# Kernel optimization log

Measured on AMD Instinct MI355X. Metric: run time of the kernel, lower is better.

## Reference

```python
import jax, jax.numpy as jnp
import numpy as np

N_HEAD = 16


def setup_inputs() -> dict:
    key = jax.random.key(0)
    ks = jax.random.split(key, 11)
    B, T, D = 8, 448, 1024
    init = 0.02
    x = jax.random.normal(ks[0], (B, T, D), dtype=jnp.float32)
    k_cache = jax.random.normal(ks[1], (B, T, D), dtype=jnp.float32)
    v_cache = jax.random.normal(ks[2], (B, T, D), dtype=jnp.float32)
    # Whisper-style additive causal mask: 0 on/below diagonal, large negative above
    mask = jnp.triu(jnp.full((T, T), -1e9, dtype=jnp.float32), k=1)
    Wq = jax.random.normal(ks[3], (D, D), dtype=jnp.float32) * init
    bq = jax.random.normal(ks[4], (D,), dtype=jnp.float32) * init
    Wk = jax.random.normal(ks[5], (D, D), dtype=jnp.float32) * init  # key proj has no bias
    Wv = jax.random.normal(ks[6], (D, D), dtype=jnp.float32) * init
    bv = jax.random.normal(ks[7], (D,), dtype=jnp.float32) * init
    Wo = jax.random.normal(ks[8], (D, D), dtype=jnp.float32) * init
    bo = jax.random.normal(ks[9], (D,), dtype=jnp.float32) * init
    return {"x": x, "k_cache": k_cache, "v_cache": v_cache, "mask": mask,
            "Wq": Wq, "bq": bq, "Wk": Wk, "Wv": Wv, "bv": bv, "Wo": Wo, "bo": bo}


def reference(x, k_cache, v_cache, mask, Wq, bq, Wk, Wv, bv, Wo, bo):
    # QKV projections (key has no bias, as in Whisper)
    q = x @ Wq + bq
    k = x @ Wk
    v = x @ Wv + bv
    # In-place KV cache append: write new keys/values into the tail of the cache
    T_new = k.shape[1]
    k_cache = k_cache.at[:, -T_new:, :].set(k)
    v_cache = v_cache.at[:, -T_new:, :].set(v)

    B, T, D = q.shape
    H = N_HEAD
    dh = D // H
    scale = dh ** (-0.25)  # applied to BOTH q and k

    qh = (q * scale).reshape(B, T, H, dh).transpose(0, 2, 1, 3)           # [B,H,T,dh]
    kh = (k_cache * scale).reshape(B, k_cache.shape[1], H, dh).transpose(0, 2, 1, 3)
    vh = v_cache.reshape(B, v_cache.shape[1], H, dh).transpose(0, 2, 1, 3)

    qk = jnp.einsum('bhqd,bhkd->bhqk', qh, kh) + mask[:T, :T]             # [B,H,T,Tc]
    qk = qk.astype(jnp.float32)  # upcast for softmax, matching original
    w = jax.nn.softmax(qk, axis=-1).astype(q.dtype)

    out = jnp.einsum('bhqk,bhkd->bhqd', w, vh)                            # [B,H,T,dh]
    out = out.transpose(0, 2, 1, 3).reshape(B, T, D)
    return out @ Wo + bo, k_cache, v_cache
```

## Files before the change

kernel.cpp:

```cpp
#include <hip/hip_runtime.h>
#include <hip/hip_bf16.h>
#include <math.h>

#define B 8
#define T 448
#define D 1024
#define H 16
#define DH 64
#define M (B*T)

typedef short short8 __attribute__((ext_vector_type(8)));
typedef float floatx4 __attribute__((ext_vector_type(4)));
typedef unsigned short u16;

__device__ __forceinline__ u16 f2bf(float f) {
    union { float f; unsigned u; } v; v.f = f;
    unsigned r = v.u + 0x7FFF + ((v.u >> 16) & 1);
    return (u16)(r >> 16);
}

__device__ __forceinline__ void gload16(const void* gptr, void* lptr) {
    __builtin_amdgcn_global_load_lds(
        (const __attribute__((address_space(1))) void*)gptr,
        (__attribute__((address_space(3))) void*)lptr, 16, 0, 0);
}

__global__ __launch_bounds__(256) void xconv(const float* __restrict__ x, u16* __restrict__ xb) {
    const int i = blockIdx.x * 256 + threadIdx.x;
    float4 v = ((const float4*)x)[i];
    ushort4 o;
    o.x = f2bf(v.x); o.y = f2bf(v.y); o.z = f2bf(v.z); o.w = f2bf(v.w);
    ((ushort4*)xb)[i] = o;
}

__global__ __launch_bounds__(256) void wconv4(
    const float* __restrict__ Wq, const float* __restrict__ Wk,
    const float* __restrict__ Wv, const float* __restrict__ Wo,
    u16* __restrict__ wt)
{
    __shared__ float tile[64][65];
    const int z = blockIdx.z;
    const float* W = (z == 0) ? Wq : (z == 1) ? Wk : (z == 2) ? Wv : Wo;
    u16* Wt = wt + (size_t)z * D * D;
    const int k0 = blockIdx.y * 64, n0 = blockIdx.x * 64;
    const int tr = threadIdx.x >> 4, tc = threadIdx.x & 15;
    #pragma unroll
    for (int i = 0; i < 4; ++i) {
        float4 v = *(const float4*)(W + (size_t)(k0 + tr + 16 * i) * D + n0 + tc * 4);
        tile[tr + 16 * i][tc * 4 + 0] = v.x;
        tile[tr + 16 * i][tc * 4 + 1] = v.y;
        tile[tr + 16 * i][tc * 4 + 2] = v.z;
        tile[tr + 16 * i][tc * 4 + 3] = v.w;
    }
    __syncthreads();
    #pragma unroll
    for (int i = 0; i < 4; ++i) {
        const int n = tr + 16 * i;
        ushort4 o;
        o.x = f2bf(tile[tc * 4 + 0][n]);
        o.y = f2bf(tile[tc * 4 + 1][n]);
        o.z = f2bf(tile[tc * 4 + 2][n]);
        o.w = f2bf(tile[tc * 4 + 3][n]);
        *(ushort4*)(Wt + (size_t)(n0 + n) * D + k0 + tc * 4) = o;
    }
}

__global__ __launch_bounds__(256) void gemm128(
    const u16* __restrict__ A, const u16* __restrict__ Bt, int mode,
    const float* __restrict__ bq, const float* __restrict__ bv,
    u16* __restrict__ qkvb, float* __restrict__ kout, float* __restrict__ vout,
    u16* __restrict__ vbT,
    const float* __restrict__ bo, float* __restrict__ outp)
{
    __shared__ u16 As[128][32];
    __shared__ u16 Bs[128][32];
    const int m0 = blockIdx.y * 128;
    const int n0 = blockIdx.x * 128;
    const int tid = threadIdx.x;
    const int wave = tid >> 6, lane = tid & 63;
    const int wy = wave >> 1, wx = wave & 1;
    const int lrow = lane & 15, lquad = lane >> 4;

    floatx4 acc[4][4];
    #pragma unroll
    for (int i = 0; i < 4; ++i)
        #pragma unroll
        for (int j = 0; j < 4; ++j)
            acc[i][j] = (floatx4){0.f, 0.f, 0.f, 0.f};

    const u16* agp0 = A + (size_t)(m0 + (tid >> 2)) * 1024 + (tid & 3) * 8;
    const u16* agp1 = agp0 + (size_t)64 * 1024;
    const u16* bgp0 = Bt + (size_t)(n0 + (tid >> 2)) * 1024 + (tid & 3) * 8;
    const u16* bgp1 = bgp0 + (size_t)64 * 1024;
    char* lA0 = (char*)&As[0][0] + wave * 1024;
    char* lA1 = lA0 + 4096;
    char* lB0 = (char*)&Bs[0][0] + wave * 1024;
    char* lB1 = lB0 + 4096;

    for (int k0 = 0; k0 < 1024; k0 += 32) {
        __syncthreads();
        gload16(agp0 + k0, lA0);
        gload16(agp1 + k0, lA1);
        gload16(bgp0 + k0, lB0);
        gload16(bgp1 + k0, lB1);
        __syncthreads();
        short8 af[4], bfr[4];
        #pragma unroll
        for (int i = 0; i < 4; ++i)
            af[i] = *(const short8*)&As[wy * 64 + i * 16 + lrow][lquad * 8];
        #pragma unroll
        for (int j = 0; j < 4; ++j)
            bfr[j] = *(const short8*)&Bs[wx * 64 + j * 16 + lrow][lquad * 8];
        #pragma unroll
        for (int i = 0; i < 4; ++i)
            #pragma unroll
            for (int j = 0; j < 4; ++j)
                acc[i][j] = __builtin_amdgcn_mfma_f32_16x16x32_bf16(af[i], bfr[j], acc[i][j], 0, 0, 0);
    }

    const int sec = (mode == 0) ? (n0 >> 10) : 3;
    #pragma unroll
    for (int j = 0; j < 4; ++j) {
        const int col = n0 + wx * 64 + j * 16 + lrow;
        float bb;
        if (mode == 1) bb = bo[col];
        else bb = (sec == 0) ? bq[col] : (sec == 2 ? bv[col - 2048] : 0.f);
        #pragma unroll
        for (int i = 0; i < 4; ++i) {
            #pragma unroll
            for (int r = 0; r < 4; ++r) {
                const int row = m0 + wy * 64 + i * 16 + lquad * 4 + r;
                const float v = acc[i][j][r] + bb;
                if (mode == 1) {
                    outp[(size_t)row * 1024 + col] = v;
                } else if (sec == 0) {
                    qkvb[(size_t)row * 3072 + col] = f2bf(v);
                } else if (sec == 1) {
                    qkvb[(size_t)row * 3072 + col] = f2bf(v);
                    kout[(size_t)row * 1024 + col - 1024] = v;
                } else {
                    vout[(size_t)row * 1024 + col - 2048] = v;
                    const int bidx = row / 448, tt = row - bidx * 448;
                    vbT[((size_t)bidx * 1024 + (col - 2048)) * 448 + tt] = f2bf(v);
                }
            }
        }
    }
}

__global__ __launch_bounds__(256) void flash_attn(
    const u16* __restrict__ QKVb,
    const u16* __restrict__ VbT,
    u16* __restrict__ Ob)
{
    __shared__ u16 Qs[64][72];
    __shared__ u16 Ks[64][72];
    __shared__ u16 Vt[64][72];
    __shared__ u16 Pt[4][16][72];
    const int qt = blockIdx.x;
    const int bh = blockIdx.y;
    const int h = bh & (H - 1), b = bh >> 4;
    const int tid = threadIdx.x, wave = tid >> 6, lane = tid & 63;
    const int lrow = lane & 15, lquad = lane >> 4;
    const int q0 = qt * 64;

    const u16* qbase = QKVb + (size_t)b * T * 3072 + (size_t)h * DH;
    const u16* kbase = qbase + 1024;
    const u16* vtb   = VbT + (size_t)bh * DH * T;

    {
        const int s = tid * 2;
        short8 v0 = *(const short8*)(qbase + (size_t)(q0 + (s >> 3)) * 3072 + (s & 7) * 8);
        short8 v1 = *(const short8*)(qbase + (size_t)(q0 + ((s + 1) >> 3)) * 3072 + ((s + 1) & 7) * 8);
        *(short8*)&Qs[s >> 3][(s & 7) * 8] = v0;
        *(short8*)&Qs[(s + 1) >> 3][((s + 1) & 7) * 8] = v1;
    }
    __syncthreads();
    short8 aq0 = *(const short8*)&Qs[wave * 16 + lrow][lquad * 8];
    short8 aq1 = *(const short8*)&Qs[wave * 16 + lrow][32 + lquad * 8];

    float m_i[4], l_i[4];
    floatx4 oacc[4];
    #pragma unroll
    for (int r = 0; r < 4; ++r) { m_i[r] = -INFINITY; l_i[r] = 0.f; }
    #pragma unroll
    for (int n = 0; n < 4; ++n) oacc[n] = (floatx4){0.f, 0.f, 0.f, 0.f};

    const float SC = 0.125f * 1.44269504088896340736f;
    const int nkt = qt + 1;

    for (int kt = 0; kt < nkt; ++kt) {
        const int k0 = kt * 64;
        {
            const int s = tid * 2;
            const int r0 = s >> 3, o0 = (s & 7) * 8;
            const int r1 = (s + 1) >> 3, o1 = ((s + 1) & 7) * 8;
            short8 kv0 = *(const short8*)(kbase + (size_t)(k0 + r0) * 3072 + o0);
            short8 kv1 = *(const short8*)(kbase + (size_t)(k0 + r1) * 3072 + o1);
            short8 vv0 = *(const short8*)(vtb + (size_t)r0 * T + k0 + o0);
            short8 vv1 = *(const short8*)(vtb + (size_t)r1 * T + k0 + o1);
            __syncthreads();
            *(short8*)&Ks[r0][o0] = kv0;
            *(short8*)&Ks[r1][o1] = kv1;
            *(short8*)&Vt[r0][o0] = vv0;
            *(short8*)&Vt[r1][o1] = vv1;
        }
        __syncthreads();

        floatx4 s4[4];
        #pragma unroll
        for (int sub = 0; sub < 4; ++sub) {
            short8 bk0 = *(const short8*)&Ks[sub * 16 + lrow][lquad * 8];
            short8 bk1 = *(const short8*)&Ks[sub * 16 + lrow][32 + lquad * 8];
            floatx4 z = (floatx4){0.f, 0.f, 0.f, 0.f};
            z = __builtin_amdgcn_mfma_f32_16x16x32_bf16(aq0, bk0, z, 0, 0, 0);
            z = __builtin_amdgcn_mfma_f32_16x16x32_bf16(aq1, bk1, z, 0, 0, 0);
            s4[sub] = z;
        }

        float p[4][4];
        #pragma unroll
        for (int r = 0; r < 4; ++r) {
            const int qg = q0 + wave * 16 + lquad * 4 + r;
            float sv[4];
            float mx = -INFINITY;
            #pragma unroll
            for (int sub = 0; sub < 4; ++sub) {
                const int kk = k0 + sub * 16 + lrow;
                float v = s4[sub][r] * SC;
                v = (kk <= qg) ? v : -INFINITY;
                sv[sub] = v;
                mx = fmaxf(mx, v);
            }
            mx = fmaxf(mx, __shfl_xor(mx, 1));
            mx = fmaxf(mx, __shfl_xor(mx, 2));
            mx = fmaxf(mx, __shfl_xor(mx, 4));
            mx = fmaxf(mx, __shfl_xor(mx, 8));
            const float mnew = fmaxf(m_i[r], mx);
            const float alpha = exp2f(m_i[r] - mnew);
            float ls = 0.f;
            #pragma unroll
            for (int sub = 0; sub < 4; ++sub) {
                const float pv = exp2f(sv[sub] - mnew);
                p[sub][r] = pv;
                ls += pv;
            }
            ls += __shfl_xor(ls, 1);
            ls += __shfl_xor(ls, 2);
            ls += __shfl_xor(ls, 4);
            ls += __shfl_xor(ls, 8);
            l_i[r] = l_i[r] * alpha + ls;
            m_i[r] = mnew;
            #pragma unroll
            for (int n = 0; n < 4; ++n) oacc[n][r] *= alpha;
        }

        #pragma unroll
        for (int sub = 0; sub < 4; ++sub)
            #pragma unroll
            for (int r = 0; r < 4; ++r)
                Pt[wave][lquad * 4 + r][sub * 16 + lrow] = f2bf(p[sub][r]);
        __syncthreads();
        short8 ap0 = *(const short8*)&Pt[wave][lrow][lquad * 8];
        short8 ap1 = *(const short8*)&Pt[wave][lrow][32 + lquad * 8];

        #pragma unroll
        for (int n = 0; n < 4; ++n) {
            short8 bv0 = *(const short8*)&Vt[n * 16 + lrow][lquad * 8];
            short8 bv1 = *(const short8*)&Vt[n * 16 + lrow][32 + lquad * 8];
            oacc[n] = __builtin_amdgcn_mfma_f32_16x16x32_bf16(ap0, bv0, oacc[n], 0, 0, 0);
            oacc[n] = __builtin_amdgcn_mfma_f32_16x16x32_bf16(ap1, bv1, oacc[n], 0, 0, 0);
        }
    }

    #pragma unroll
    for (int r = 0; r < 4; ++r) {
        const float inv = 1.f / l_i[r];
        const int qg = q0 + wave * 16 + lquad * 4 + r;
        u16* orow = Ob + ((size_t)b * T + qg) * D + (size_t)h * DH;
        #pragma unroll
        for (int n = 0; n < 4; ++n)
            orow[n * 16 + lrow] = f2bf(oacc[n][r] * inv);
    }
}

extern "C" void kernel_launch(void* const* d_in, const int* in_sizes, int n_in,
                              void* d_out, int out_size, void* d_ws, size_t ws_size,
                              hipStream_t stream) {
    const float* x  = (const float*)d_in[0];
    const float* Wq = (const float*)d_in[4];
    const float* bq = (const float*)d_in[5];
    const float* Wk = (const float*)d_in[6];
    const float* Wv = (const float*)d_in[7];
    const float* bv = (const float*)d_in[8];
    const float* Wo = (const float*)d_in[9];
    const float* bo = (const float*)d_in[10];

    float* out  = (float*)d_out;
    float* kout = out + (size_t)M * D;
    float* vout = out + 2 * (size_t)M * D;

    u16* xb   = (u16*)d_ws;
    u16* wt   = xb   + (size_t)M * D;
    u16* qkvb = wt   + (size_t)4 * D * D;
    u16* vbT  = qkvb + (size_t)M * 3 * D;
    u16* ab   = vbT  + (size_t)M * D;

    xconv<<<M * D / 1024, 256, 0, stream>>>(x, xb);
    wconv4<<<dim3(16, 16, 4), 256, 0, stream>>>(Wq, Wk, Wv, Wo, wt);

    gemm128<<<dim3(24, 28), 256, 0, stream>>>(xb, wt, 0, bq, bv,
                                              qkvb, kout, vout, vbT, nullptr, nullptr);

    flash_attn<<<dim3(7, 128), 256, 0, stream>>>(qkvb, vbT, ab);

    gemm128<<<dim3(8, 28), 256, 0, stream>>>(ab, wt + (size_t)3 * D * D, 1, nullptr, nullptr,
                                             nullptr, nullptr, nullptr, nullptr, bo, out);
}
```

Measured before the change: 210.3 us.

## Shrink GEMM tile to 64x128 with two waves and deeper K step

Replaces the 128x128 four-wave GEMM block with a 64x128 two-wave block and doubles the K step per iteration to 64, halving the number of barrier pairs. This doubles the grid size (672 and 224 blocks) so the 256-CU device gets more blocks per launch, especially for the output projection. The cost is less A/B reuse per block, so more global and L2 traffic, and more loads in flight per thread.

```diff
diff --git a/kernel.cpp b/kernel.cpp
--- a/kernel.cpp
+++ b/kernel.cpp
@@ -65,20 +65,19 @@
     }
 }
 
-__global__ __launch_bounds__(256) void gemm128(
+__global__ __launch_bounds__(128) void gemm64(
     const u16* __restrict__ A, const u16* __restrict__ Bt, int mode,
     const float* __restrict__ bq, const float* __restrict__ bv,
     u16* __restrict__ qkvb, float* __restrict__ kout, float* __restrict__ vout,
     u16* __restrict__ vbT,
     const float* __restrict__ bo, float* __restrict__ outp)
 {
-    __shared__ u16 As[128][32];
-    __shared__ u16 Bs[128][32];
-    const int m0 = blockIdx.y * 128;
+    __shared__ u16 As[2][64][32];
+    __shared__ u16 Bs[2][128][32];
+    const int m0 = blockIdx.y * 64;
     const int n0 = blockIdx.x * 128;
     const int tid = threadIdx.x;
     const int wave = tid >> 6, lane = tid & 63;
-    const int wy = wave >> 1, wx = wave & 1;
     const int lrow = lane & 15, lquad = lane >> 4;
 
     floatx4 acc[4][4];
@@ -88,40 +87,49 @@
         for (int j = 0; j < 4; ++j)
             acc[i][j] = (floatx4){0.f, 0.f, 0.f, 0.f};
 
-    const u16* agp0 = A + (size_t)(m0 + (tid >> 2)) * 1024 + (tid & 3) * 8;
-    const u16* agp1 = agp0 + (size_t)64 * 1024;
-    const u16* bgp0 = Bt + (size_t)(n0 + (tid >> 2)) * 1024 + (tid & 3) * 8;
-    const u16* bgp1 = bgp0 + (size_t)64 * 1024;
-    char* lA0 = (char*)&As[0][0] + wave * 1024;
-    char* lA1 = lA0 + 4096;
-    char* lB0 = (char*)&Bs[0][0] + wave * 1024;
-    char* lB1 = lB0 + 4096;
-
-    for (int k0 = 0; k0 < 1024; k0 += 32) {
+    const u16* agp[4];
+    #pragma unroll
+    for (int i = 0; i < 4; ++i)
+        agp[i] = A + (size_t)(m0 + (i & 1) * 32 + (tid >> 2)) * 1024
+                   + (i >> 1) * 32 + (tid & 3) * 8;
+    const u16* bgp[8];
+    #pragma unroll
+    for (int i = 0; i < 8; ++i)
+        bgp[i] = Bt + (size_t)(n0 + (i & 3) * 32 + (tid >> 2)) * 1024
+                    + (i >> 2) * 32 + (tid & 3) * 8;
+    char* lA = (char*)&As[0][0][0] + wave * 1024;
+    char* lB = (char*)&Bs[0][0][0] + wave * 1024;
+
+    for (int k0 = 0; k0 < 1024; k0 += 64) {
         __syncthreads();
-        gload16(agp0 + k0, lA0);
-        gload16(agp1 + k0, lA1);
-        gload16(bgp0 + k0, lB0);
-        gload16(bgp1 + k0, lB1);
+        #pragma unroll
+        for (int i = 0; i < 4; ++i) gload16(agp[i] + k0, lA + i * 2048);
+        #pragma unroll
+        for (int i = 0; i < 8; ++i) gload16(bgp[i] + k0, lB + i * 2048);
         __syncthreads();
-        short8 af[4], bfr[4];
-        #pragma unroll
-        for (int i = 0; i < 4; ++i)
-            af[i] = *(const short8*)&As[wy * 64 + i * 16 + lrow][lquad * 8];
-        #pragma unroll
-        for (int j = 0; j < 4; ++j)
-            bfr[j] = *(const short8*)&Bs[wx * 64 + j * 16 + lrow][lquad * 8];
-        #pragma unroll
-        for (int i = 0; i < 4; ++i)
+        short8 af[4][2], bfr[4][2];
+        #pragma unroll
+        for (int s = 0; s < 2; ++s) {
+            #pragma unroll
+            for (int i = 0; i < 4; ++i)
+                af[i][s] = *(const short8*)&As[s][i * 16 + lrow][lquad * 8];
             #pragma unroll
             for (int j = 0; j < 4; ++j)
-                acc[i][j] = __builtin_amdgcn_mfma_f32_16x16x32_bf16(af[i], bfr[j], acc[i][j], 0, 0, 0);
+                bfr[j][s] = *(const short8*)&Bs[s][wave * 64 + j * 16 + lrow][lquad * 8];
+        }
+        #pragma unroll
+        for (int s = 0; s < 2; ++s)
+            #pragma unroll
+            for (int i = 0; i < 4; ++i)
+                #pragma unroll
+                for (int j = 0; j < 4; ++j)
+                    acc[i][j] = __builtin_amdgcn_mfma_f32_16x16x32_bf16(af[i][s], bfr[j][s], acc[i][j], 0, 0, 0);
     }
 
     const int sec = (mode == 0) ? (n0 >> 10) : 3;
     #pragma unroll
     for (int j = 0; j < 4; ++j) {
-        const int col = n0 + wx * 64 + j * 16 + lrow;
+        const int col = n0 + wave * 64 + j * 16 + lrow;
         float bb;
         if (mode == 1) bb = bo[col];
         else bb = (sec == 0) ? bq[col] : (sec == 2 ? bv[col - 2048] : 0.f);
@@ -129,7 +137,7 @@
         for (int i = 0; i < 4; ++i) {
             #pragma unroll
             for (int r = 0; r < 4; ++r) {
-                const int row = m0 + wy * 64 + i * 16 + lquad * 4 + r;
+                const int row = m0 + i * 16 + lquad * 4 + r;
                 const float v = acc[i][j][r] + bb;
                 if (mode == 1) {
                     outp[(size_t)row * 1024 + col] = v;
@@ -309,11 +317,11 @@
     xconv<<<M * D / 1024, 256, 0, stream>>>(x, xb);
     wconv4<<<dim3(16, 16, 4), 256, 0, stream>>>(Wq, Wk, Wv, Wo, wt);
 
-    gemm128<<<dim3(24, 28), 256, 0, stream>>>(xb, wt, 0, bq, bv,
-                                              qkvb, kout, vout, vbT, nullptr, nullptr);
+    gemm64<<<dim3(24, 56), 128, 0, stream>>>(xb, wt, 0, bq, bv,
+                                             qkvb, kout, vout, vbT, nullptr, nullptr);
 
     flash_attn<<<dim3(7, 128), 256, 0, stream>>>(qkvb, vbT, ab);
 
-    gemm128<<<dim3(8, 28), 256, 0, stream>>>(ab, wt + (size_t)3 * D * D, 1, nullptr, nullptr,
-                                             nullptr, nullptr, nullptr, nullptr, bo, out);
-}
+    gemm64<<<dim3(8, 56), 128, 0, stream>>>(ab, wt + (size_t)3 * D * D, 1, nullptr, nullptr,
+                                            nullptr, nullptr, nullptr, nullptr, bo, out);
+}
```

Result: slower. 224.5 us (+6.8%).
